# Performance work log

Measured on AMD Instinct MI355X. Metric: run time of the kernel, lower is better.

Reference implementation:

```python
import jax, jax.numpy as jnp
import numpy as np

N = 100000
E = 1600000
IN, HID, OUT = 768, 128, 64


def gcn_conv(x, W, b, src, dst, num_nodes):
    """PyG GCNConv: linear transform, add self-loops, symmetric norm, scatter-add, bias."""
    xw = x @ W  # [N, C_out] (transform before aggregation, as PyG does)
    loops = jnp.arange(num_nodes, dtype=src.dtype)
    s = jnp.concatenate([src, loops])
    d = jnp.concatenate([dst, loops])
    deg = jax.ops.segment_sum(jnp.ones_like(d, dtype=xw.dtype), d, num_segments=num_nodes)
    dis = jnp.where(deg > 0, jax.lax.rsqrt(deg), 0.0)
    norm = dis[s] * dis[d]  # [E+N]
    msg = xw[s] * norm[:, None]  # gather + scale
    out = jax.ops.segment_sum(msg, d, num_segments=num_nodes)  # scatter-add
    return out + b


def setup_inputs() -> dict:
    key = jax.random.key(0)
    ks = jax.random.split(key, 6)
    x = jax.random.normal(ks[0], (N, IN), dtype=jnp.float32)
    edge_index = jax.random.randint(ks[1], (2, E), 0, N, dtype=jnp.int64)
    # Glorot-ish init for GCN weights, zero bias (PyG defaults)
    W1 = jax.random.normal(ks[2], (IN, HID), dtype=jnp.float32) * (1.0 / np.sqrt(IN))
    b1 = jnp.zeros((HID,), dtype=jnp.float32)
    W2 = jax.random.normal(ks[3], (HID, OUT), dtype=jnp.float32) * (1.0 / np.sqrt(HID))
    b2 = jnp.zeros((OUT,), dtype=jnp.float32)
    return {"x": x, "edge_index": edge_index, "W1": W1, "b1": b1, "W2": W2, "b2": b2}


def reference(x, edge_index, W1, b1, W2, b2):
    src, dst = edge_index[0], edge_index[1]
    h = jax.nn.relu(gcn_conv(x, W1, b1, src, dst, N))
    z = gcn_conv(h, W2, b2, src, dst, N)
    return z
```

## Files before the change

kernel.cpp:

```cpp
#include <hip/hip_runtime.h>
#include <hip/hip_bf16.h>


static constexpr int NN    = 100000;
static constexpr int NE    = 1600000;
static constexpr int C_IN  = 768;
static constexpr int C_HID = 128;
static constexpr int C_OUT = 64;
static constexpr int SCAN_B = 256;
static constexpr int NB_SCAN = (NN + SCAN_B - 1) / SCAN_B;

__global__ void k_zero_i(int* __restrict__ p, int n) {
    int i = blockIdx.x * blockDim.x + threadIdx.x;
    if (i < n) p[i] = 0;
}

__global__ void k_hist(const int* __restrict__ dst, int* __restrict__ cnt, int e) {
    int stride = gridDim.x * blockDim.x;
    for (int i = blockIdx.x * blockDim.x + threadIdx.x; i < e; i += stride)
        atomicAdd(&cnt[dst[i]], 1);
}

__global__ void k_dis(const int* __restrict__ cnt, float* __restrict__ dis, int n) {
    int i = blockIdx.x * blockDim.x + threadIdx.x;
    if (i < n) dis[i] = rsqrtf((float)cnt[i] + 1.0f);
}

__global__ __launch_bounds__(SCAN_B) void k_scan1(const int* __restrict__ cnt,
                                                  int* __restrict__ rp1,
                                                  int* __restrict__ bsum, int n) {
    __shared__ int sh[SCAN_B];
    int b = blockIdx.x, t = threadIdx.x, i = b * SCAN_B + t;
    sh[t] = (i < n) ? cnt[i] : 0;
    __syncthreads();
    for (int off = 1; off < SCAN_B; off <<= 1) {
        int u = (t >= off) ? sh[t - off] : 0;
        __syncthreads();
        sh[t] += u;
        __syncthreads();
    }
    if (i < n) rp1[i] = sh[t];
    if (t == SCAN_B - 1) bsum[b] = sh[t];
}

__global__ __launch_bounds__(512) void k_scan2(int* __restrict__ bsum, int nb) {
    __shared__ int sh[512];
    int t = threadIdx.x;
    sh[t] = (t < nb) ? bsum[t] : 0;
    __syncthreads();
    for (int off = 1; off < 512; off <<= 1) {
        int u = (t >= off) ? sh[t - off] : 0;
        __syncthreads();
        sh[t] += u;
        __syncthreads();
    }
    if (t < nb) bsum[t] = sh[t];
}

__global__ __launch_bounds__(SCAN_B) void k_scan3(int* __restrict__ rowptr,
                                                  const int* __restrict__ bsum,
                                                  int* __restrict__ cursor, int n) {
    int b = blockIdx.x, t = threadIdx.x, i = b * SCAN_B + t;
    if (b == 0 && t == 0) { rowptr[0] = 0; cursor[0] = 0; }
    if (i < n) {
        int v = rowptr[1 + i] + (b > 0 ? bsum[b - 1] : 0);
        rowptr[1 + i] = v;
        if (i + 1 < n) cursor[i + 1] = v;
    }
}

__global__ void k_scatter(const int* __restrict__ src, const int* __restrict__ dst,
                          int* __restrict__ cursor, int* __restrict__ csr, int e) {
    int stride = gridDim.x * blockDim.x;
    for (int i = blockIdx.x * blockDim.x + threadIdx.x; i < e; i += stride) {
        int p = atomicAdd(&cursor[dst[i]], 1);
        csr[p] = src[i];
    }
}

template<int K, int N>
__global__ __launch_bounds__(256) void k_gemm(const float* __restrict__ A,
                                              const float* __restrict__ B,
                                              float* __restrict__ C,
                                              const float* __restrict__ dis, int M) {
    constexpr int BM = 64, BK = 32;
    constexpr int CPT = N / 16;
    __shared__ float sA[BK][BM + 4];
    __shared__ float sB[BK][N];

    const int tid  = threadIdx.x;
    const int row0 = blockIdx.x * BM;
    const int tr   = tid >> 4;
    const int tc   = tid & 15;

    float acc[4][CPT];
    #pragma unroll
    for (int i = 0; i < 4; ++i)
        #pragma unroll
        for (int j = 0; j < CPT; ++j) acc[i][j] = 0.f;

    for (int k0 = 0; k0 < K; k0 += BK) {
        #pragma unroll
        for (int l = 0; l < 2; ++l) {
            int t  = tid + l * 256;
            int r  = t >> 3;
            int cc = (t & 7) << 2;
            int gr = row0 + r;
            float4 v = make_float4(0.f, 0.f, 0.f, 0.f);
            if (gr < M) v = *(const float4*)(A + gr * K + k0 + cc);
            sA[cc + 0][r] = v.x; sA[cc + 1][r] = v.y;
            sA[cc + 2][r] = v.z; sA[cc + 3][r] = v.w;
        }
        #pragma unroll
        for (int l = 0; l < (8 * N) / 256; ++l) {
            int t  = tid + l * 256;
            int r  = t / (N / 4);
            int cc = (t % (N / 4)) << 2;
            *(float4*)(&sB[r][cc]) = *(const float4*)(B + (k0 + r) * N + cc);
        }
        __syncthreads();
        #pragma unroll
        for (int k = 0; k < BK; ++k) {
            float a[4], b[CPT];
            *(float4*)a = *(const float4*)(&sA[k][tr * 4]);
            #pragma unroll
            for (int j = 0; j < CPT; j += 4)
                *(float4*)(&b[j]) = *(const float4*)(&sB[k][tc * CPT + j]);
            #pragma unroll
            for (int i = 0; i < 4; ++i)
                #pragma unroll
                for (int j = 0; j < CPT; ++j)
                    acc[i][j] += a[i] * b[j];
        }
        __syncthreads();
    }
    #pragma unroll
    for (int i = 0; i < 4; ++i) {
        int row = row0 + tr * 4 + i;
        if (row < M) {
            float dn = dis[row];
            #pragma unroll
            for (int j = 0; j < CPT; ++j) acc[i][j] *= dn;
            #pragma unroll
            for (int j = 0; j < CPT; j += 4)
                *(float4*)(C + row * N + tc * CPT + j) = *(float4*)(&acc[i][j]);
        }
    }
}

template<int C, bool RELU>
__global__ __launch_bounds__(C) void k_agg(const int* __restrict__ rowptr,
                                           const int* __restrict__ csr,
                                           const float* __restrict__ feat,
                                           const float* __restrict__ dis,
                                           const float* __restrict__ bias,
                                           float* __restrict__ out) {
    const int d = blockIdx.x;
    const int c = threadIdx.x;
    const int beg = rowptr[d], end = rowptr[d + 1];
    float sum = feat[d * C + c];
    int e = beg;
    for (; e + 4 <= end; e += 4) {
        int s0 = csr[e], s1 = csr[e + 1], s2 = csr[e + 2], s3 = csr[e + 3];
        float f0 = feat[s0 * C + c], f1 = feat[s1 * C + c];
        float f2 = feat[s2 * C + c], f3 = feat[s3 * C + c];
        sum += (f0 + f1) + (f2 + f3);
    }
    for (; e < end; ++e) sum += feat[csr[e] * C + c];
    float r = sum * dis[d] + bias[c];
    if (RELU) r = fmaxf(r, 0.f);
    out[d * C + c] = r;
}

extern "C" void kernel_launch(void* const* d_in, const int* in_sizes, int n_in,
                              void* d_out, int out_size, void* d_ws, size_t ws_size,
                              hipStream_t stream) {
    const float* x  = (const float*)d_in[0];
    const int*   ei = (const int*)d_in[1];
    const float* W1 = (const float*)d_in[2];
    const float* b1 = (const float*)d_in[3];
    const float* W2 = (const float*)d_in[4];
    const float* b2 = (const float*)d_in[5];
    float* z = (float*)d_out;

    char* ws = (char*)d_ws;
    float* dis    = (float*)(ws + 0);
    int*   cnt    = (int*)  (ws + 524288);
    int*   rowptr = (int*)  (ws + 1048576);
    int*   bsum   = (int*)  (ws + 1572864);
    int*   csr    = (int*)  (ws + 2097152);
    float* xw     = (float*)(ws + 8912896);
    float* h      = (float*)(ws + 60817408);

    const int* src = ei;
    const int* dst = ei + NE;

    k_zero_i<<<(NN + 255) / 256, 256, 0, stream>>>(cnt, NN);
    k_hist<<<4096, 256, 0, stream>>>(dst, cnt, NE);
    k_dis<<<(NN + 255) / 256, 256, 0, stream>>>(cnt, dis, NN);
    k_scan1<<<NB_SCAN, SCAN_B, 0, stream>>>(cnt, rowptr + 1, bsum, NN);
    k_scan2<<<1, 512, 0, stream>>>(bsum, NB_SCAN);
    k_scan3<<<NB_SCAN, SCAN_B, 0, stream>>>(rowptr, bsum, cnt , NN);
    k_scatter<<<4096, 256, 0, stream>>>(src, dst, cnt , csr, NE);

    k_gemm<C_IN, C_HID><<<(NN + 63) / 64, 256, 0, stream>>>(x, W1, xw, dis, NN);
    k_agg<C_HID, true><<<NN, C_HID, 0, stream>>>(rowptr, csr, xw, dis, b1, h);

    float* hw = xw;
    k_gemm<C_HID, C_OUT><<<(NN + 63) / 64, 256, 0, stream>>>(h, W2, hw, dis, NN);
    k_agg<C_OUT, false><<<NN, C_OUT, 0, stream>>>(rowptr, csr, hw, dis, b2, z);
}
```

Baseline: 990.5 us.

## Replace FP32 SIMT GEMMs with split-bf16 MFMA GEMMs (3-term hi/lo)

After: 895.5 us. 1.11x faster.

```diff
diff --git a/kernel.cpp b/kernel.cpp
--- a/kernel.cpp
+++ b/kernel.cpp
@@ -9,6 +9,18 @@
 static constexpr int C_OUT = 64;
 static constexpr int SCAN_B = 256;
 static constexpr int NB_SCAN = (NN + SCAN_B - 1) / SCAN_B;
+
+typedef __attribute__((ext_vector_type(8))) short bf16x8;
+typedef __attribute__((ext_vector_type(4))) float f32x4;
+
+__device__ __forceinline__ unsigned short f2bf(float f) {
+    unsigned int x = __float_as_uint(f);
+    unsigned int r = (x + 0x7fffu + ((x >> 16) & 1u)) >> 16;
+    return (unsigned short)r;
+}
+__device__ __forceinline__ float bf2f(unsigned short u) {
+    return __uint_as_float(((unsigned int)u) << 16);
+}
 
 __global__ void k_zero_i(int* __restrict__ p, int n) {
     int i = blockIdx.x * blockDim.x + threadIdx.x;
@@ -79,71 +91,109 @@
 }
 
 template<int K, int N>
-__global__ __launch_bounds__(256) void k_gemm(const float* __restrict__ A,
-                                              const float* __restrict__ B,
-                                              float* __restrict__ C,
-                                              const float* __restrict__ dis, int M) {
-    constexpr int BM = 64, BK = 32;
-    constexpr int CPT = N / 16;
-    __shared__ float sA[BK][BM + 4];
-    __shared__ float sB[BK][N];
+__global__ void k_splitW(const float* __restrict__ W,
+                         unsigned short* __restrict__ th,
+                         unsigned short* __restrict__ tl) {
+    int idx = blockIdx.x * blockDim.x + threadIdx.x;
+    if (idx < K * N) {
+        int k = idx / N, n = idx - k * N;
+        float a = W[idx];
+        unsigned short h = f2bf(a);
+        th[n * K + k] = h;
+        tl[n * K + k] = f2bf(a - bf2f(h));
+    }
+}
+
+template<int K, int N_>
+__global__ __launch_bounds__(256) void k_gemm_mfma(const float* __restrict__ A,
+                                                   const unsigned short* __restrict__ Bh,
+                                                   const unsigned short* __restrict__ Bl,
+                                                   float* __restrict__ C,
+                                                   const float* __restrict__ dis, int M) {
+    constexpr int RT = (N_ == 128) ? 4 : 2;
+    constexpr int CT = 2;
+    constexpr int LDK = 40;
+
+    __shared__ unsigned short sAh[64][LDK], sAl[64][LDK];
+    __shared__ unsigned short sBh[N_][LDK], sBl[N_][LDK];
 
     const int tid  = threadIdx.x;
-    const int row0 = blockIdx.x * BM;
-    const int tr   = tid >> 4;
-    const int tc   = tid & 15;
-
-    float acc[4][CPT];
+    const int w    = tid >> 6;
+    const int lane = tid & 63;
+    const int lr   = lane & 15;
+    const int ls   = lane >> 4;
+    const int row0 = blockIdx.x * 64;
+
+    const int row_base = (N_ == 128) ? 0 : (w >> 1) * 32;
+    const int col_base = (N_ == 128) ? w * 32 : (w & 1) * 32;
+
+    f32x4 acc[RT][CT];
     #pragma unroll
-    for (int i = 0; i < 4; ++i)
-        #pragma unroll
-        for (int j = 0; j < CPT; ++j) acc[i][j] = 0.f;
-
-    for (int k0 = 0; k0 < K; k0 += BK) {
+    for (int i = 0; i < RT; ++i)
+        #pragma unroll
+        for (int j = 0; j < CT; ++j) acc[i][j] = (f32x4){0.f, 0.f, 0.f, 0.f};
+
+    for (int k0 = 0; k0 < K; k0 += 32) {
         #pragma unroll
         for (int l = 0; l < 2; ++l) {
-            int t  = tid + l * 256;
-            int r  = t >> 3;
-            int cc = (t & 7) << 2;
-            int gr = row0 + r;
+            int f   = tid + l * 256;
+            int row = f >> 3;
+            int kc  = (f & 7) << 2;
+            int gr  = row0 + row;
             float4 v = make_float4(0.f, 0.f, 0.f, 0.f);
-            if (gr < M) v = *(const float4*)(A + gr * K + k0 + cc);
-            sA[cc + 0][r] = v.x; sA[cc + 1][r] = v.y;
-            sA[cc + 2][r] = v.z; sA[cc + 3][r] = v.w;
-        }
-        #pragma unroll
-        for (int l = 0; l < (8 * N) / 256; ++l) {
-            int t  = tid + l * 256;
-            int r  = t / (N / 4);
-            int cc = (t % (N / 4)) << 2;
-            *(float4*)(&sB[r][cc]) = *(const float4*)(B + (k0 + r) * N + cc);
-        }
-        __syncthreads();
-        #pragma unroll
-        for (int k = 0; k < BK; ++k) {
-            float a[4], b[CPT];
-            *(float4*)a = *(const float4*)(&sA[k][tr * 4]);
+            if (gr < M) v = *(const float4*)(A + gr * K + k0 + kc);
+            unsigned short h0 = f2bf(v.x), h1 = f2bf(v.y), h2 = f2bf(v.z), h3 = f2bf(v.w);
+            *(short4*)&sAh[row][kc] = make_short4(h0, h1, h2, h3);
+            *(short4*)&sAl[row][kc] = make_short4(f2bf(v.x - bf2f(h0)), f2bf(v.y - bf2f(h1)),
+                                                  f2bf(v.z - bf2f(h2)), f2bf(v.w - bf2f(h3)));
+        }
+        #pragma unroll
+        for (int l = 0; l < (N_ * 4) / 256; ++l) {
+            int c   = tid + l * 256;
+            int col = c >> 2;
+            int kc8 = (c & 3) * 8;
+            *(uint4*)&sBh[col][kc8] = *(const uint4*)&Bh[col * K + k0 + kc8];
+            *(uint4*)&sBl[col][kc8] = *(const uint4*)&Bl[col * K + k0 + kc8];
+        }
+        __syncthreads();
+
+        bf16x8 ah[RT], al[RT], bh[CT], bl[CT];
+        #pragma unroll
+        for (int rt = 0; rt < RT; ++rt) {
+            int arow = row_base + rt * 16 + lr;
+            ah[rt] = *(const bf16x8*)&sAh[arow][ls * 8];
+            al[rt] = *(const bf16x8*)&sAl[arow][ls * 8];
+        }
+        #pragma unroll
+        for (int ct = 0; ct < CT; ++ct) {
+            int bcol = col_base + ct * 16 + lr;
+            bh[ct] = *(const bf16x8*)&sBh[bcol][ls * 8];
+            bl[ct] = *(const bf16x8*)&sBl[bcol][ls * 8];
+        }
+        #pragma unroll
+        for (int rt = 0; rt < RT; ++rt)
             #pragma unroll
-            for (int j = 0; j < CPT; j += 4)
-                *(float4*)(&b[j]) = *(const float4*)(&sB[k][tc * CPT + j]);
-            #pragma unroll
-            for (int i = 0; i < 4; ++i)
+            for (int ct = 0; ct < CT; ++ct) {
+                acc[rt][ct] = __builtin_amdgcn_mfma_f32_16x16x32_bf16(ah[rt], bh[ct], acc[rt][ct], 0, 0, 0);
+                acc[rt][ct] = __builtin_amdgcn_mfma_f32_16x16x32_bf16(ah[rt], bl[ct], acc[rt][ct], 0, 0, 0);
+                acc[rt][ct] = __builtin_amdgcn_mfma_f32_16x16x32_bf16(al[rt], bh[ct], acc[rt][ct], 0, 0, 0);
+            }
+        __syncthreads();
+    }
+
+    #pragma unroll
+    for (int rt = 0; rt < RT; ++rt) {
+        #pragma unroll
+        for (int r = 0; r < 4; ++r) {
+            int grow = row0 + row_base + rt * 16 + ls * 4 + r;
+            if (grow < M) {
+                float dn = dis[grow];
                 #pragma unroll
-                for (int j = 0; j < CPT; ++j)
-                    acc[i][j] += a[i] * b[j];
-        }
-        __syncthreads();
-    }
-    #pragma unroll
-    for (int i = 0; i < 4; ++i) {
-        int row = row0 + tr * 4 + i;
-        if (row < M) {
-            float dn = dis[row];
-            #pragma unroll
-            for (int j = 0; j < CPT; ++j) acc[i][j] *= dn;
-            #pragma unroll
-            for (int j = 0; j < CPT; j += 4)
-                *(float4*)(C + row * N + tc * CPT + j) = *(float4*)(&acc[i][j]);
+                for (int ct = 0; ct < CT; ++ct) {
+                    int gcol = col_base + ct * 16 + lr;
+                    C[grow * N_ + gcol] = acc[rt][ct][r] * dn;
+                }
+            }
         }
     }
 }
@@ -189,7 +239,11 @@
     int*   rowptr = (int*)  (ws + 1048576);
     int*   bsum   = (int*)  (ws + 1572864);
     int*   csr    = (int*)  (ws + 2097152);
-    float* xw     = (float*)(ws + 8912896);
+    unsigned short* w1h = (unsigned short*)(ws + 8912896);
+    unsigned short* w1l = (unsigned short*)(ws + 9109504);
+    unsigned short* w2h = (unsigned short*)(ws + 9306112);
+    unsigned short* w2l = (unsigned short*)(ws + 9322496);
+    float* xw     = (float*)(ws + 9437184);
     float* h      = (float*)(ws + 60817408);
 
     const int* src = ei;
@@ -203,10 +257,13 @@
     k_scan3<<<NB_SCAN, SCAN_B, 0, stream>>>(rowptr, bsum, cnt , NN);
     k_scatter<<<4096, 256, 0, stream>>>(src, dst, cnt , csr, NE);
 
-    k_gemm<C_IN, C_HID><<<(NN + 63) / 64, 256, 0, stream>>>(x, W1, xw, dis, NN);
+    k_splitW<C_IN, C_HID><<<(C_IN * C_HID + 255) / 256, 256, 0, stream>>>(W1, w1h, w1l);
+    k_splitW<C_HID, C_OUT><<<(C_HID * C_OUT + 255) / 256, 256, 0, stream>>>(W2, w2h, w2l);
+
+    k_gemm_mfma<C_IN, C_HID><<<(NN + 63) / 64, 256, 0, stream>>>(x, w1h, w1l, xw, dis, NN);
     k_agg<C_HID, true><<<NN, C_HID, 0, stream>>>(rowptr, csr, xw, dis, b1, h);
 
     float* hw = xw;
-    k_gemm<C_HID, C_OUT><<<(NN + 63) / 64, 256, 0, stream>>>(h, W2, hw, dis, NN);
+    k_gemm_mfma<C_HID, C_OUT><<<(NN + 63) / 64, 256, 0, stream>>>(h, w2h, w2l, hw, dis, NN);
     k_agg<C_OUT, false><<<NN, C_OUT, 0, stream>>>(rowptr, csr, hw, dis, b2, z);
 }
```
